# Kernel tuning notes

Measured on AMD Instinct MI355X. Metric: run time of the kernel, lower is better.

## Reference

```python
import jax, jax.numpy as jnp
import numpy as np

EMBED_DIM = 1024
MEMORY_SIZE = 64
TOPK = 3
LN_EPS = 1e-5


def setup_inputs() -> dict:
    key = jax.random.key(0)
    ks = jax.random.split(key, 8)
    D, M = EMBED_DIM, MEMORY_SIZE
    scale = 1.0 / np.sqrt(D)
    x = jax.random.normal(ks[0], (8, 2048, D), dtype=jnp.float32)
    memory = jax.random.normal(ks[1], (M, D), dtype=jnp.float32) * scale
    Wq = jax.random.normal(ks[2], (D, D), dtype=jnp.float32) * scale
    bq = jnp.zeros((D,), dtype=jnp.float32)
    Wf = jax.random.normal(ks[3], (D, 2 * D), dtype=jnp.float32) * (1.0 / np.sqrt(2 * D))
    bf = jnp.zeros((D,), dtype=jnp.float32)
    gamma = jnp.ones((D,), dtype=jnp.float32)
    beta = jnp.zeros((D,), dtype=jnp.float32)
    return {"x": x, "memory": memory, "Wq": Wq, "bq": bq,
            "Wf": Wf, "bf": bf, "gamma": gamma, "beta": beta}


def reference(x, memory, Wq, bq, Wf, bf, gamma, beta):
    B, S, D = x.shape
    # query projection: [B,S,D]
    query = jnp.einsum('bsd,ed->bse', x, Wq) + bq
    # similarity to memory bank: [B,S,M]
    sim = jnp.einsum('bsd,md->bsm', query, memory)
    # top-k over memory slots
    topk_sim, topk_idx = jax.lax.top_k(sim, TOPK)            # [B,S,K]
    weights = jax.nn.softmax(topk_sim, axis=-1)               # [B,S,K]
    retrieved = memory[topk_idx]                              # [B,S,K,D]
    memory_output = jnp.einsum('bskd,bsk->bsd', retrieved, weights)
    # fusion MLP: Linear(2D->D) -> LayerNorm -> ReLU
    cat = jnp.concatenate([x, memory_output], axis=-1)        # [B,S,2D]
    h = jnp.einsum('bsc,dc->bsd', cat, Wf) + bf
    mean = jnp.mean(h, axis=-1, keepdims=True)
    var = jnp.mean(jnp.square(h - mean), axis=-1, keepdims=True)
    h = (h - mean) * jax.lax.rsqrt(var + LN_EPS) * gamma + beta
    return jax.nn.relu(h)
```

## Files before the change

### kernel.cpp

```cpp
#include <hip/hip_runtime.h>

#define DCH 1024
#define MSLOT 64
#define NTOK 16384

typedef __bf16 bf16x8 __attribute__((ext_vector_type(8)));
typedef float f32x4 __attribute__((ext_vector_type(4)));
typedef unsigned short u16x8 __attribute__((ext_vector_type(8)));
typedef unsigned short u16x4 __attribute__((ext_vector_type(4)));

__device__ __forceinline__ unsigned short f2bf(float f) {
  unsigned u = __float_as_uint(f);
  u += 0x7fffu + ((u >> 16) & 1u);
  return (unsigned short)(u >> 16);
}
__device__ __forceinline__ float bf2f(unsigned short s) {
  return __uint_as_float(((unsigned)s) << 16);
}

__device__ __forceinline__ void gld16(const void* g, void* l) {
  __builtin_amdgcn_global_load_lds((const __attribute__((address_space(1))) void*)g,
                                   (__attribute__((address_space(3))) void*)l, 16, 0, 0);
}

__global__ __launch_bounds__(256) void prep_a_kernel(
    const float* __restrict__ x, unsigned short* __restrict__ xb,
    const float* __restrict__ Wf, float* __restrict__ Wf2T,
    unsigned short* __restrict__ Wf1b,
    const float* __restrict__ bq, const float* __restrict__ memv,
    float* __restrict__ sc) {
  __shared__ float tile[64][65];
  __shared__ float red[256];
  const int b = blockIdx.x, tid = threadIdx.x;

  if (b < 8192) {
    int idx8 = (b * 256 + tid) * 8;
    float4 a = *(const float4*)(x + idx8);
    float4 c = *(const float4*)(x + idx8 + 4);
    u16x8 o = {f2bf(a.x), f2bf(a.y), f2bf(a.z), f2bf(a.w),
               f2bf(c.x), f2bf(c.y), f2bf(c.z), f2bf(c.w)};
    *(u16x8*)(xb + idx8) = o;
  } else if (b < 8448) {
    const int t = b - 8192;
    const int c0 = (t & 15) * 64, d0 = (t >> 4) * 64;
    const int lane = tid & 63, wv = tid >> 6;
#pragma unroll
    for (int i = 0; i < 16; ++i) {
      int r = wv + i * 4;
      tile[r][lane] = Wf[(size_t)(d0 + r) * 2048 + 1024 + c0 + lane];
    }
    __syncthreads();
#pragma unroll
    for (int i = 0; i < 16; ++i) {
      int r = wv + i * 4;
      Wf2T[(size_t)(c0 + r) * 1024 + d0 + lane] = tile[lane][r];
    }
  } else if (b < 8512) {
    const int j = b - 8448;
#pragma unroll
    for (int i = 0; i < 16; ++i) {
      int f4 = j * 4096 + i * 256 + tid;
      int row = f4 >> 8, c4 = (f4 & 255) * 4;
      float4 v = *(const float4*)(Wf + (size_t)row * 2048 + c4);
      u16x4 o = {f2bf(v.x), f2bf(v.y), f2bf(v.z), f2bf(v.w)};
      *(u16x4*)(Wf1b + row * 1024 + c4) = o;
    }
  } else {
    int m = tid >> 2, q = tid & 3;
    float s = 0.f;
    for (int e = q * 256; e < q * 256 + 256; ++e) s += bq[e] * memv[m * 1024 + e];
    red[tid] = s;
    __syncthreads();
    if (tid < 64) sc[tid] = red[tid * 4] + red[tid * 4 + 1] + red[tid * 4 + 2] + red[tid * 4 + 3];
  }
}

__global__ __launch_bounds__(256) void prep_b_kernel(
    const float* __restrict__ memv, const float* __restrict__ Wq,
    const float* __restrict__ Wf2T,
    float* __restrict__ partWm, float* __restrict__ partP) {
  int b = blockIdx.x;
  const int tid = threadIdx.x;
  const int which = b >> 7;
  b &= 127;
  const int kc = b & 7, dt = (b >> 3) & 3, mg = b >> 5;
  const float* B = which ? Wf2T : Wq;
  float* outp = which ? partP : partWm;
  const int d = dt * 256 + tid;
  const int e0 = kc * 128;
  const int m0 = mg * 16;

  float acc[16];
#pragma unroll
  for (int m = 0; m < 16; ++m) acc[m] = 0.f;

  const float* bp = B + (size_t)e0 * 1024 + d;
  const float* mp = memv + m0 * 1024 + e0;
#pragma unroll 4
  for (int e = 0; e < 128; ++e) {
    float wv = bp[(size_t)e * 1024];
#pragma unroll
    for (int m = 0; m < 16; ++m) acc[m] += mp[m * 1024 + e] * wv;
  }
  float* op = outp + ((size_t)kc * 64 + m0) * 1024 + d;
#pragma unroll
  for (int m = 0; m < 16; ++m) op[m * 1024] = acc[m];
}

__global__ __launch_bounds__(256) void prep_c_kernel(
    const float* __restrict__ partWm, const float* __restrict__ partP,
    unsigned short* __restrict__ Wmb, float* __restrict__ P) {
  int idx = blockIdx.x * 256 + threadIdx.x;
  if (idx < 65536) {
    float s = 0.f;
#pragma unroll
    for (int k = 0; k < 8; ++k) s += partWm[k * 65536 + idx];
    Wmb[idx] = f2bf(s);
  } else {
    idx -= 65536;
    float s = 0.f;
#pragma unroll
    for (int k = 0; k < 8; ++k) s += partP[k * 65536 + idx];
    P[idx] = s;
  }
}

__global__ __launch_bounds__(256) void sim_topk_kernel(
    const unsigned short* __restrict__ xb, const unsigned short* __restrict__ Wmb,
    const float* __restrict__ sc, float4* __restrict__ meta) {
  __shared__ __attribute__((aligned(16))) unsigned short As[128 * 64];
  __shared__ __attribute__((aligned(16))) unsigned short Bs[64 * 64];
  __shared__ float sim_s[128 * 65];
  const int tid = threadIdx.x;
  const int wave = tid >> 6, lane = tid & 63;
  const int tok0 = blockIdx.x * 128;
  const int quad = lane >> 4, cl = lane & 15;

  f32x4 acc[2][4];
#pragma unroll
  for (int i = 0; i < 2; ++i)
#pragma unroll
    for (int j = 0; j < 4; ++j) acc[i][j] = {0.f, 0.f, 0.f, 0.f};

  for (int kt = 0; kt < 16; ++kt) {
    __syncthreads();
#pragma unroll
    for (int i = 0; i < 4; ++i) {
      int ch = (wave * 4 + i) * 64 + lane;
      int row = ch >> 3, cb = (ch & 7) * 8;
      gld16(xb + (size_t)(tok0 + row) * 1024 + kt * 64 + cb, As + ch * 8);
    }
#pragma unroll
    for (int i = 0; i < 2; ++i) {
      int ch = (wave * 2 + i) * 64 + lane;
      int row = ch >> 3, cb = (ch & 7) * 8;
      gld16(Wmb + row * 1024 + kt * 64 + cb, Bs + ch * 8);
    }
    __syncthreads();
    const unsigned short* Ab = As + (wave * 32 + cl) * 64 + quad * 8;
    const unsigned short* Bb = Bs + cl * 64 + quad * 8;
#pragma unroll
    for (int ks = 0; ks < 2; ++ks) {
      bf16x8 a0 = *(const bf16x8*)(Ab + ks * 32);
      bf16x8 a1 = *(const bf16x8*)(Ab + 16 * 64 + ks * 32);
#pragma unroll
      for (int nt = 0; nt < 4; ++nt) {
        bf16x8 bb = *(const bf16x8*)(Bb + nt * 16 * 64 + ks * 32);
        acc[0][nt] = __builtin_amdgcn_mfma_f32_16x16x32_bf16(a0, bb, acc[0][nt], 0, 0, 0);
        acc[1][nt] = __builtin_amdgcn_mfma_f32_16x16x32_bf16(a1, bb, acc[1][nt], 0, 0, 0);
      }
    }
  }
#pragma unroll
  for (int mt = 0; mt < 2; ++mt)
#pragma unroll
    for (int nt = 0; nt < 4; ++nt)
#pragma unroll
      for (int r = 0; r < 4; ++r) {
        int lt = wave * 32 + mt * 16 + quad * 4 + r;
        int mc = nt * 16 + cl;
        sim_s[lt * 65 + mc] = acc[mt][nt][r] + sc[mc];
      }
  __syncthreads();
  if (tid < 128) {
    const float* sp = sim_s + tid * 65;
    float s0 = -1e30f, s1 = -1e30f, s2 = -1e30f;
    int i0 = 0, i1 = 0, i2 = 0;
    for (int m = 0; m < 64; ++m) {
      float v = sp[m];
      if (v > s0) { s2 = s1; i2 = i1; s1 = s0; i1 = i0; s0 = v; i0 = m; }
      else if (v > s1) { s2 = s1; i2 = i1; s1 = v; i1 = m; }
      else if (v > s2) { s2 = v; i2 = m; }
    }
    float e1 = __expf(s1 - s0), e2 = __expf(s2 - s0);
    float inv = 1.f / (1.f + e1 + e2);
    meta[tok0 + tid] = make_float4(inv, e1 * inv, e2 * inv,
                                   __int_as_float(i0 | (i1 << 8) | (i2 << 16)));
  }
}

__global__ __launch_bounds__(256) void gemm_h_kernel(
    const unsigned short* __restrict__ xb, const unsigned short* __restrict__ Wf1b,
    const float* __restrict__ P, const float4* __restrict__ meta,
    const float* __restrict__ bfv, unsigned short* __restrict__ hb) {
  __shared__ __attribute__((aligned(16))) unsigned short As[128 * 64];
  __shared__ __attribute__((aligned(16))) unsigned short Bs[128 * 64];
  const int tid = threadIdx.x;
  const int wave = tid >> 6, lane = tid & 63;
  const int d0 = blockIdx.x * 128, tok0 = blockIdx.y * 128;
  const int quad = lane >> 4, cl = lane & 15;
  const int wm = (wave & 1) * 64, wn = (wave >> 1) * 64;

  f32x4 acc[4][4];
#pragma unroll
  for (int i = 0; i < 4; ++i)
#pragma unroll
    for (int j = 0; j < 4; ++j) acc[i][j] = {0.f, 0.f, 0.f, 0.f};

  for (int kt = 0; kt < 16; ++kt) {
    __syncthreads();
#pragma unroll
    for (int i = 0; i < 4; ++i) {
      int ch = (wave * 4 + i) * 64 + lane;
      int row = ch >> 3, cb = (ch & 7) * 8;
      gld16(xb + (size_t)(tok0 + row) * 1024 + kt * 64 + cb, As + ch * 8);
      gld16(Wf1b + (size_t)(d0 + row) * 1024 + kt * 64 + cb, Bs + ch * 8);
    }
    __syncthreads();
    const unsigned short* Ab = As + (wm + cl) * 64 + quad * 8;
    const unsigned short* Bb = Bs + (wn + cl) * 64 + quad * 8;
#pragma unroll
    for (int ks = 0; ks < 2; ++ks) {
      bf16x8 a[4], b[4];
#pragma unroll
      for (int t = 0; t < 4; ++t) a[t] = *(const bf16x8*)(Ab + t * 1024 + ks * 32);
#pragma unroll
      for (int t = 0; t < 4; ++t) b[t] = *(const bf16x8*)(Bb + t * 1024 + ks * 32);
#pragma unroll
      for (int mt = 0; mt < 4; ++mt)
#pragma unroll
        for (int nt = 0; nt < 4; ++nt)
          acc[mt][nt] = __builtin_amdgcn_mfma_f32_16x16x32_bf16(a[mt], b[nt], acc[mt][nt], 0, 0, 0);
    }
  }

#pragma unroll
  for (int mt = 0; mt < 4; ++mt) {
#pragma unroll
    for (int r = 0; r < 4; ++r) {
      int row = tok0 + wm + mt * 16 + quad * 4 + r;
      float4 mv = meta[row];
      int pk = __float_as_int(mv.w);
      const float* P0 = P + (pk & 255) * 1024;
      const float* P1 = P + ((pk >> 8) & 255) * 1024;
      const float* P2 = P + ((pk >> 16) & 255) * 1024;
#pragma unroll
      for (int nt = 0; nt < 4; ++nt) {
        int d = d0 + wn + nt * 16 + cl;
        float h = acc[mt][nt][r] + bfv[d] + mv.x * P0[d] + mv.y * P1[d] + mv.z * P2[d];
        hb[(size_t)row * 1024 + d] = f2bf(h);
      }
    }
  }
}

__global__ __launch_bounds__(256) void ln_relu_kernel(
    const unsigned short* __restrict__ hb, const float* __restrict__ gamma,
    const float* __restrict__ beta, float* __restrict__ out) {
  const int tid = threadIdx.x;
  const int wave = tid >> 6, lane = tid & 63;
  const int t = blockIdx.x * 4 + wave;
  const unsigned short* hp = hb + (size_t)t * 1024 + lane * 16;
  u16x8 h0 = *(const u16x8*)(hp);
  u16x8 h1 = *(const u16x8*)(hp + 8);
  float f[16];
#pragma unroll
  for (int j = 0; j < 8; ++j) { f[j] = bf2f(h0[j]); f[8 + j] = bf2f(h1[j]); }
  float s = 0.f, q = 0.f;
#pragma unroll
  for (int j = 0; j < 16; ++j) { s += f[j]; q += f[j] * f[j]; }
#pragma unroll
  for (int off = 32; off; off >>= 1) {
    s += __shfl_xor(s, off);
    q += __shfl_xor(q, off);
  }
  float mean = s * (1.f / 1024.f);
  float var = q * (1.f / 1024.f) - mean * mean;
  float rs = rsqrtf(var + 1e-5f);
  const int dbase = lane * 16;
  float o[16];
#pragma unroll
  for (int j = 0; j < 16; ++j) {
    float v = (f[j] - mean) * rs * gamma[dbase + j] + beta[dbase + j];
    o[j] = fmaxf(v, 0.f);
  }
  float* op = out + (size_t)t * 1024 + dbase;
#pragma unroll
  for (int j4 = 0; j4 < 4; ++j4) {
    float4 v = {o[j4 * 4], o[j4 * 4 + 1], o[j4 * 4 + 2], o[j4 * 4 + 3]};
    *(float4*)(op + j4 * 4) = v;
  }
}

extern "C" void kernel_launch(void* const* d_in, const int* in_sizes, int n_in,
                              void* d_out, int out_size, void* d_ws, size_t ws_size,
                              hipStream_t stream) {
  const float* x     = (const float*)d_in[0];
  const float* memv  = (const float*)d_in[1];
  const float* Wq    = (const float*)d_in[2];
  const float* bq    = (const float*)d_in[3];
  const float* Wf    = (const float*)d_in[4];
  const float* bfv   = (const float*)d_in[5];
  const float* gamma = (const float*)d_in[6];
  const float* beta  = (const float*)d_in[7];
  float* out = (float*)d_out;
  char* ws = (char*)d_ws;

  unsigned short* Wf1b   = (unsigned short*)(ws);
  unsigned short* Wmb    = (unsigned short*)(ws + 2097152);
  float*          P      = (float*)(ws + 2228224);
  float*          sc     = (float*)(ws + 2490368);
  float4*         meta   = (float4*)(ws + 2490624);
  float*          Wf2T   = (float*)(ws + 2752768);
  float*          partWm = (float*)(ws + 6947072);
  float*          partP  = (float*)(ws + 9044224);
  unsigned short* xb     = (unsigned short*)(ws + 11141376);
  unsigned short* hb     = (unsigned short*)(ws + 44695808);

  hipLaunchKernelGGL(prep_a_kernel, dim3(8513), dim3(256), 0, stream,
                     x, xb, Wf, Wf2T, Wf1b, bq, memv, sc);
  hipLaunchKernelGGL(prep_b_kernel, dim3(256), dim3(256), 0, stream,
                     memv, Wq, Wf2T, partWm, partP);
  hipLaunchKernelGGL(prep_c_kernel, dim3(512), dim3(256), 0, stream,
                     partWm, partP, Wmb, P);
  hipLaunchKernelGGL(sim_topk_kernel, dim3(128), dim3(256), 0, stream,
                     xb, Wmb, sc, meta);
  hipLaunchKernelGGL(gemm_h_kernel, dim3(8, 128), dim3(256), 0, stream,
                     xb, Wf1b, P, meta, bfv, hb);
  hipLaunchKernelGGL(ln_relu_kernel, dim3(4096), dim3(256), 0, stream,
                     hb, gamma, beta, out);
}
```

Before: 283.7 us.

## Move memory-term epilogue into LayerNorm kernel and retile sim/gemm grids

The top-k memory contribution (bias plus weighted rows of P) moves from the GEMM epilogue into the LayerNorm kernel. There it is read as contiguous float4 loads per token instead of scattered scalar loads inside the MFMA epilogue. This leaves the GEMM epilogue a plain store, but hb now holds the pre-bias value rounded to bf16 before the memory term is added, which slightly changes rounding. The sim_topk kernel now uses 64-token tiles and 256 blocks to fill more CUs. The GEMM grid is flattened so consecutive blocks walk tokens while sharing a weight column tile, which may improve L2 reuse of Wf1b.

```diff
diff --git a/kernel.cpp b/kernel.cpp
--- a/kernel.cpp
+++ b/kernel.cpp
@@ -128,61 +128,50 @@
 __global__ __launch_bounds__(256) void sim_topk_kernel(
     const unsigned short* __restrict__ xb, const unsigned short* __restrict__ Wmb,
     const float* __restrict__ sc, float4* __restrict__ meta) {
-  __shared__ __attribute__((aligned(16))) unsigned short As[128 * 64];
+  __shared__ __attribute__((aligned(16))) unsigned short As[64 * 64];
   __shared__ __attribute__((aligned(16))) unsigned short Bs[64 * 64];
-  __shared__ float sim_s[128 * 65];
+  __shared__ float sim_s[64 * 65];
   const int tid = threadIdx.x;
   const int wave = tid >> 6, lane = tid & 63;
-  const int tok0 = blockIdx.x * 128;
+  const int tok0 = blockIdx.x * 64;
   const int quad = lane >> 4, cl = lane & 15;
 
-  f32x4 acc[2][4];
-#pragma unroll
-  for (int i = 0; i < 2; ++i)
-#pragma unroll
-    for (int j = 0; j < 4; ++j) acc[i][j] = {0.f, 0.f, 0.f, 0.f};
+  f32x4 acc[4];
+#pragma unroll
+  for (int j = 0; j < 4; ++j) acc[j] = {0.f, 0.f, 0.f, 0.f};
 
   for (int kt = 0; kt < 16; ++kt) {
     __syncthreads();
-#pragma unroll
-    for (int i = 0; i < 4; ++i) {
-      int ch = (wave * 4 + i) * 64 + lane;
-      int row = ch >> 3, cb = (ch & 7) * 8;
-      gld16(xb + (size_t)(tok0 + row) * 1024 + kt * 64 + cb, As + ch * 8);
-    }
 #pragma unroll
     for (int i = 0; i < 2; ++i) {
       int ch = (wave * 2 + i) * 64 + lane;
       int row = ch >> 3, cb = (ch & 7) * 8;
+      gld16(xb + (size_t)(tok0 + row) * 1024 + kt * 64 + cb, As + ch * 8);
       gld16(Wmb + row * 1024 + kt * 64 + cb, Bs + ch * 8);
     }
     __syncthreads();
-    const unsigned short* Ab = As + (wave * 32 + cl) * 64 + quad * 8;
+    const unsigned short* Ab = As + (wave * 16 + cl) * 64 + quad * 8;
     const unsigned short* Bb = Bs + cl * 64 + quad * 8;
 #pragma unroll
     for (int ks = 0; ks < 2; ++ks) {
-      bf16x8 a0 = *(const bf16x8*)(Ab + ks * 32);
-      bf16x8 a1 = *(const bf16x8*)(Ab + 16 * 64 + ks * 32);
+      bf16x8 a = *(const bf16x8*)(Ab + ks * 32);
 #pragma unroll
       for (int nt = 0; nt < 4; ++nt) {
         bf16x8 bb = *(const bf16x8*)(Bb + nt * 16 * 64 + ks * 32);
-        acc[0][nt] = __builtin_amdgcn_mfma_f32_16x16x32_bf16(a0, bb, acc[0][nt], 0, 0, 0);
-        acc[1][nt] = __builtin_amdgcn_mfma_f32_16x16x32_bf16(a1, bb, acc[1][nt], 0, 0, 0);
+        acc[nt] = __builtin_amdgcn_mfma_f32_16x16x32_bf16(a, bb, acc[nt], 0, 0, 0);
       }
     }
   }
 #pragma unroll
-  for (int mt = 0; mt < 2; ++mt)
-#pragma unroll
-    for (int nt = 0; nt < 4; ++nt)
-#pragma unroll
-      for (int r = 0; r < 4; ++r) {
-        int lt = wave * 32 + mt * 16 + quad * 4 + r;
-        int mc = nt * 16 + cl;
-        sim_s[lt * 65 + mc] = acc[mt][nt][r] + sc[mc];
-      }
+  for (int nt = 0; nt < 4; ++nt)
+#pragma unroll
+    for (int r = 0; r < 4; ++r) {
+      int lt = wave * 16 + quad * 4 + r;
+      int mc = nt * 16 + cl;
+      sim_s[lt * 65 + mc] = acc[nt][r] + sc[mc];
+    }
   __syncthreads();
-  if (tid < 128) {
+  if (tid < 64) {
     const float* sp = sim_s + tid * 65;
     float s0 = -1e30f, s1 = -1e30f, s2 = -1e30f;
     int i0 = 0, i1 = 0, i2 = 0;
@@ -201,13 +190,13 @@
 
 __global__ __launch_bounds__(256) void gemm_h_kernel(
     const unsigned short* __restrict__ xb, const unsigned short* __restrict__ Wf1b,
-    const float* __restrict__ P, const float4* __restrict__ meta,
-    const float* __restrict__ bfv, unsigned short* __restrict__ hb) {
+    unsigned short* __restrict__ hb) {
   __shared__ __attribute__((aligned(16))) unsigned short As[128 * 64];
   __shared__ __attribute__((aligned(16))) unsigned short Bs[128 * 64];
   const int tid = threadIdx.x;
   const int wave = tid >> 6, lane = tid & 63;
-  const int d0 = blockIdx.x * 128, tok0 = blockIdx.y * 128;
+  const int b = blockIdx.x;
+  const int tok0 = (b & 127) * 128, d0 = (b >> 7) * 128;
   const int quad = lane >> 4, cl = lane & 15;
   const int wm = (wave & 1) * 64, wn = (wave >> 1) * 64;
 
@@ -231,16 +220,16 @@
     const unsigned short* Bb = Bs + (wn + cl) * 64 + quad * 8;
 #pragma unroll
     for (int ks = 0; ks < 2; ++ks) {
-      bf16x8 a[4], b[4];
+      bf16x8 a[4], bb[4];
 #pragma unroll
       for (int t = 0; t < 4; ++t) a[t] = *(const bf16x8*)(Ab + t * 1024 + ks * 32);
 #pragma unroll
-      for (int t = 0; t < 4; ++t) b[t] = *(const bf16x8*)(Bb + t * 1024 + ks * 32);
+      for (int t = 0; t < 4; ++t) bb[t] = *(const bf16x8*)(Bb + t * 1024 + ks * 32);
 #pragma unroll
       for (int mt = 0; mt < 4; ++mt)
 #pragma unroll
         for (int nt = 0; nt < 4; ++nt)
-          acc[mt][nt] = __builtin_amdgcn_mfma_f32_16x16x32_bf16(a[mt], b[nt], acc[mt][nt], 0, 0, 0);
+          acc[mt][nt] = __builtin_amdgcn_mfma_f32_16x16x32_bf16(a[mt], bb[nt], acc[mt][nt], 0, 0, 0);
     }
   }
 
@@ -249,33 +238,49 @@
 #pragma unroll
     for (int r = 0; r < 4; ++r) {
       int row = tok0 + wm + mt * 16 + quad * 4 + r;
-      float4 mv = meta[row];
-      int pk = __float_as_int(mv.w);
-      const float* P0 = P + (pk & 255) * 1024;
-      const float* P1 = P + ((pk >> 8) & 255) * 1024;
-      const float* P2 = P + ((pk >> 16) & 255) * 1024;
 #pragma unroll
       for (int nt = 0; nt < 4; ++nt) {
         int d = d0 + wn + nt * 16 + cl;
-        float h = acc[mt][nt][r] + bfv[d] + mv.x * P0[d] + mv.y * P1[d] + mv.z * P2[d];
-        hb[(size_t)row * 1024 + d] = f2bf(h);
+        hb[(size_t)row * 1024 + d] = f2bf(acc[mt][nt][r]);
       }
     }
   }
 }
 
 __global__ __launch_bounds__(256) void ln_relu_kernel(
-    const unsigned short* __restrict__ hb, const float* __restrict__ gamma,
-    const float* __restrict__ beta, float* __restrict__ out) {
+    const unsigned short* __restrict__ hb, const float* __restrict__ P,
+    const float4* __restrict__ meta, const float* __restrict__ bfv,
+    const float* __restrict__ gamma, const float* __restrict__ beta,
+    float* __restrict__ out) {
   const int tid = threadIdx.x;
   const int wave = tid >> 6, lane = tid & 63;
   const int t = blockIdx.x * 4 + wave;
-  const unsigned short* hp = hb + (size_t)t * 1024 + lane * 16;
+  const int dbase = lane * 16;
+
+  float4 mv = meta[t];
+  int pk = __float_as_int(mv.w);
+  const float* P0 = P + (pk & 255) * 1024 + dbase;
+  const float* P1 = P + ((pk >> 8) & 255) * 1024 + dbase;
+  const float* P2 = P + ((pk >> 16) & 255) * 1024 + dbase;
+  const float* bp = bfv + dbase;
+
+  const unsigned short* hp = hb + (size_t)t * 1024 + dbase;
   u16x8 h0 = *(const u16x8*)(hp);
   u16x8 h1 = *(const u16x8*)(hp + 8);
   float f[16];
 #pragma unroll
   for (int j = 0; j < 8; ++j) { f[j] = bf2f(h0[j]); f[8 + j] = bf2f(h1[j]); }
+#pragma unroll
+  for (int j4 = 0; j4 < 4; ++j4) {
+    float4 b4 = *(const float4*)(bp + j4 * 4);
+    float4 p0 = *(const float4*)(P0 + j4 * 4);
+    float4 p1 = *(const float4*)(P1 + j4 * 4);
+    float4 p2 = *(const float4*)(P2 + j4 * 4);
+    f[j4 * 4 + 0] += b4.x + mv.x * p0.x + mv.y * p1.x + mv.z * p2.x;
+    f[j4 * 4 + 1] += b4.y + mv.x * p0.y + mv.y * p1.y + mv.z * p2.y;
+    f[j4 * 4 + 2] += b4.z + mv.x * p0.z + mv.y * p1.z + mv.z * p2.z;
+    f[j4 * 4 + 3] += b4.w + mv.x * p0.w + mv.y * p1.w + mv.z * p2.w;
+  }
   float s = 0.f, q = 0.f;
 #pragma unroll
   for (int j = 0; j < 16; ++j) { s += f[j]; q += f[j] * f[j]; }
@@ -287,7 +292,6 @@
   float mean = s * (1.f / 1024.f);
   float var = q * (1.f / 1024.f) - mean * mean;
   float rs = rsqrtf(var + 1e-5f);
-  const int dbase = lane * 16;
   float o[16];
 #pragma unroll
   for (int j = 0; j < 16; ++j) {
@@ -333,10 +337,10 @@
                      memv, Wq, Wf2T, partWm, partP);
   hipLaunchKernelGGL(prep_c_kernel, dim3(512), dim3(256), 0, stream,
                      partWm, partP, Wmb, P);
-  hipLaunchKernelGGL(sim_topk_kernel, dim3(128), dim3(256), 0, stream,
+  hipLaunchKernelGGL(sim_topk_kernel, dim3(256), dim3(256), 0, stream,
                      xb, Wmb, sc, meta);
-  hipLaunchKernelGGL(gemm_h_kernel, dim3(8, 128), dim3(256), 0, stream,
-                     xb, Wf1b, P, meta, bfv, hb);
+  hipLaunchKernelGGL(gemm_h_kernel, dim3(1024), dim3(256), 0, stream,
+                     xb, Wf1b, hb);
   hipLaunchKernelGGL(ln_relu_kernel, dim3(4096), dim3(256), 0, stream,
-                     hb, gamma, beta, out);
-}
+                     hb, P, meta, bfv, gamma, beta, out);
+}
```

Result: no change. 280.9 us (-1.0%).
